# Kernel tuning notes

Hardware: AMD Instinct MI355X
Metric: run time of the kernel (lower is better)

The kernel has to match this reference:

```python
import jax, jax.numpy as jnp
import numpy as np

NEG_INF = -1.0e12  # matches torch's -1e12 mask value
LEAKY_SLOPE = 0.01  # nn.LeakyReLU default


def setup_inputs() -> dict:
    key = jax.random.key(0)
    k1, k2, k3, k4 = jax.random.split(key, 4)
    B, N, in_c, out_c = 8, 2048, 64, 64
    inp = jax.random.normal(k1, (B, N, in_c), dtype=jnp.float32)
    adj = jax.random.randint(k2, (B, N, N), 0, 2, dtype=jnp.int32)
    W = jax.random.normal(k3, (in_c, out_c), dtype=jnp.float32) * (1.0 / np.sqrt(in_c))
    a = jax.random.normal(k4, (2 * out_c, 1), dtype=jnp.float32) * 0.1
    return {"inp": inp, "adj": adj, "W": W, "a": a}


def reference(inp, adj, W, a):
    # GAT layer. The original builds an O(B*N^2*2*out_c) concat tensor;
    # a^T [h_i || h_j] decomposes exactly into (h_i . a1) + (h_j . a2).
    out_c = W.shape[1]
    h = jnp.einsum('bni,io->bno', inp, W)          # [B,N,out_c]
    a1 = a[:out_c, 0]                               # [out_c]
    a2 = a[out_c:, 0]                               # [out_c]
    e_i = h @ a1                                    # [B,N] source term
    e_j = h @ a2                                    # [B,N] target term
    e = e_i[:, :, None] + e_j[:, None, :]           # [B,N,N]
    e = jnp.where(e > 0, e, LEAKY_SLOPE * e)        # LeakyReLU(0.01)
    masked = jnp.where(adj > 0, e, NEG_INF)
    attention = jax.nn.softmax(masked, axis=2)      # [B,N,N]
    # dropout omitted (eval mode / deterministic reference)
    h_prime = jnp.einsum('bnm,bmo->bno', attention, h)  # [B,N,out_c]
    return h_prime
```

## Files before the change

kernel.cpp:

```cpp
#include <hip/hip_runtime.h>
#include <cstdint>

#define BB 8
#define NN 2048
#define CC 64
#define TI 64
#define JCH 128
#define NCH 8

typedef __attribute__((ext_vector_type(8))) _Float16 f16x8;
typedef __attribute__((ext_vector_type(4))) float f32x4;
typedef __attribute__((ext_vector_type(4))) unsigned int u32x4;
typedef __attribute__((ext_vector_type(4))) int i32x4;

static const size_t WS_H   = 0;
static const size_t WS_E1  = WS_H  + (size_t)BB*NN*CC;
static const size_t WS_E2  = WS_E1 + (size_t)BB*NN;
static const size_t WS_HT  = WS_E2 + (size_t)BB*NN;

#define GL16(g, l) __builtin_amdgcn_global_load_lds( \
    (const __attribute__((address_space(1))) void*)(g), \
    (__attribute__((address_space(3))) void*)(uint32_t)(uintptr_t)(l), 16, 0, 0)
#define GL4(g, l) __builtin_amdgcn_global_load_lds( \
    (const __attribute__((address_space(1))) void*)(g), \
    (__attribute__((address_space(3))) void*)(uint32_t)(uintptr_t)(l), 4, 0, 0)
#define WAIT14() asm volatile("s_waitcnt vmcnt(14)" ::: "memory")
#define WAIT0()  asm volatile("s_waitcnt vmcnt(0)" ::: "memory")
#define BAR()    __builtin_amdgcn_s_barrier()

__global__ __launch_bounds__(256) void k1_proj(const float* __restrict__ inp,
        const float* __restrict__ Wm, const float* __restrict__ av,
        float* __restrict__ h, float* __restrict__ e1, float* __restrict__ e2) {
    __shared__ float inp_lds[256];
    int t = threadIdx.x;
    size_t base = (size_t)blockIdx.x * 256;
    inp_lds[t] = inp[base + t];
    __syncthreads();
    int r = t >> 6;
    int c = t & 63;
    const float* irow = &inp_lds[r * 64];
    float acc = 0.f;
    #pragma unroll
    for (int k = 0; k < 64; k++) acc = fmaf(irow[k], Wm[k * 64 + c], acc);
    size_t row = (size_t)blockIdx.x * 4 + r;
    h[row * 64 + c] = acc;
    float v1 = acc * av[c];
    float v2 = acc * av[64 + c];
    #pragma unroll
    for (int o = 32; o > 0; o >>= 1) {
        v1 += __shfl_down(v1, o);
        v2 += __shfl_down(v2, o);
    }
    if (c == 0) { e1[row] = v1; e2[row] = v2; }
}

__global__ __launch_bounds__(256) void k1b_transpose(const float* __restrict__ h,
        unsigned short* __restrict__ hT) {
    __shared__ float tile[64][65];
    int t = threadIdx.x;
    int b = blockIdx.x >> 5;
    int i0 = (blockIdx.x & 31) * 64;
    const float* hb = h + ((size_t)b * NN + i0) * CC;
    #pragma unroll
    for (int q = 0; q < 16; q++) {
        int idx = q * 256 + t;
        tile[idx >> 6][idx & 63] = hb[idx];
    }
    __syncthreads();
    int c = t & 63;
    int rgrp = t >> 6;
    unsigned int uh[8];
    #pragma unroll
    for (int p = 0; p < 8; p++) {
        unsigned int pack_h = 0;
        #pragma unroll
        for (int s = 0; s < 2; s++) {
            float v = tile[rgrp * 16 + p * 2 + s][c];
            _Float16 fh = (_Float16)v;
            unsigned int u = (unsigned int)__builtin_bit_cast(unsigned short, fh);
            pack_h |= u << (16 * s);
        }
        uh[p] = pack_h;
    }
    size_t off = ((size_t)b * 64 + c) * NN + i0 + rgrp * 16;
    u32x4* dh = (u32x4*)(hT + off);
    dh[0] = u32x4{uh[0], uh[1], uh[2], uh[3]};
    dh[1] = u32x4{uh[4], uh[5], uh[6], uh[7]};
}

__global__ __launch_bounds__(512, 1) void k2_mfma(const int* __restrict__ adj,
        const unsigned short* __restrict__ hT,
        const float* __restrict__ e1, const float* __restrict__ e2,
        float* __restrict__ out) {
    __shared__ __align__(16) char smem[84224];

    int bid = blockIdx.x;
    int b    = bid & 7;
    int tile = bid >> 3;
    int i0 = tile * TI;

    int t = threadIdx.x;
    int w = t >> 6;
    int hw = w >> 2;
    int wl = w & 3;
    int l = t & 63;
    int col = l & 15;
    int kg  = l >> 4;
    int jbase = hw * 1024;

    int sl  = l & 15;
    int half_off = hw * 32768;

    const int* adjrow = adj + ((size_t)b * NN + i0 + wl * 16 + col) * NN;
    float e1v = e1[(size_t)b * NN + i0 + wl * 16 + col];
    const float* e2b = e2 + (size_t)b * NN;
    const unsigned short* hTb = hT + (size_t)b * 64 * NN;

    f32x4 acc[4];
    #pragma unroll
    for (int n = 0; n < 4; n++) acc[n] = f32x4{0.f, 0.f, 0.f, 0.f};
    f32x4 accZ = f32x4{0.f, 0.f, 0.f, 0.f};

    _Float16 onev = (_Float16)1.0f, zerov = (_Float16)0.0f;
    f16x8 onesf;
    #pragma unroll
    for (int i = 0; i < 8; i++) onesf[i] = (col == 0) ? onev : zerov;

    i32x4 aA[8], aB[8];

#define STAGE(jcN, B) { \
    int j0s = jbase + (jcN) * JCH; \
    char* lb = smem + half_off + ((B) ? 16384 : 0) + wl * 4096; \
    _Pragma("unroll") \
    for (int q = 0; q < 4; q++) { \
        int c = wl * 16 + q * 4 + (l >> 4); \
        const unsigned short* src = hTb + (size_t)c * NN + j0s + ((sl ^ (c & 7)) << 3); \
        GL16(src, lb + q * 1024); \
    } \
    char* e2d = smem + 65536 + hw * 1024 + ((B) ? 512 : 0); \
    GL4(e2b + j0s + l, e2d); \
    GL4(e2b + j0s + 64 + l, e2d + 256); \
}

#define ADJP(jcN, arr) { \
    int j0a = jbase + (jcN) * JCH; \
    _Pragma("unroll") \
    for (int ks = 0; ks < 4; ks++) { \
        const i32x4* ap = (const i32x4*)(adjrow + j0a + ks * 32 + kg * 8); \
        arr[2 * ks]     = ap[0]; \
        arr[2 * ks + 1] = ap[1]; \
    } \
}

#define COMPUTE(B, arr) { \
    const char* hLb = smem + half_off + ((B) ? 16384 : 0); \
    const float* e2c = (const float*)(smem + 65536 + hw * 1024 + ((B) ? 512 : 0)); \
    _Pragma("unroll") \
    for (int ks = 0; ks < 4; ks++) { \
        int krel = ks * 32 + kg * 8; \
        i32x4 a0 = arr[2 * ks]; \
        i32x4 a1 = arr[2 * ks + 1]; \
        f32x4 e20 = *(const f32x4*)(e2c + krel); \
        f32x4 e21 = *(const f32x4*)(e2c + krel + 4); \
        float xs[8] = {e20.x, e20.y, e20.z, e20.w, e21.x, e21.y, e21.z, e21.w}; \
        int ms[8] = {a0.x, a0.y, a0.z, a0.w, a1.x, a1.y, a1.z, a1.w}; \
        f16x8 pf; \
        _Pragma("unroll") \
        for (int i = 0; i < 8; i++) { \
            float x = e1v + xs[i]; \
            x = fmaxf(x, 0.01f * x); \
            x = __expf(x); \
            x = (ms[i] > 0) ? x : 0.0f; \
            pf[i] = (_Float16)x; \
        } \
        int seg = ks * 4 + kg; \
        _Pragma("unroll") \
        for (int n = 0; n < 4; n++) { \
            int c = n * 16 + col; \
            int boff = c * 256 + ((seg ^ (c & 7)) << 4); \
            f16x8 hv = __builtin_bit_cast(f16x8, *(const f32x4*)(hLb + boff)); \
            acc[n] = __builtin_amdgcn_mfma_f32_16x16x32_f16(pf, hv, acc[n], 0, 0, 0); \
        } \
        accZ = __builtin_amdgcn_mfma_f32_16x16x32_f16(pf, onesf, accZ, 0, 0, 0); \
    } \
}

    STAGE(0, 0);
    ADJP(0, aA);

    #pragma unroll
    for (int jc = 0; jc < NCH; jc += 2) {
        STAGE(jc + 1, 1);
        ADJP(jc + 1, aB);
        WAIT14();
        BAR();
        COMPUTE(0, aA);
        BAR();
        if (jc + 2 < NCH) {
            STAGE(jc + 2, 0);
            ADJP(jc + 2, aA);
            WAIT14();
        } else {
            WAIT0();
        }
        BAR();
        COMPUTE(1, aB);
        BAR();
    }

    float* red  = (float*)(smem + 67584 + wl * 4096);
    float* zred = (float*)(smem + 83968);
    if (hw == 1) {
        #pragma unroll
        for (int n = 0; n < 4; n++)
            #pragma unroll
            for (int r = 0; r < 4; r++)
                red[(kg * 4 + r) * 64 + n * 16 + col] = acc[n][r];
        if (col == 0) {
            #pragma unroll
            for (int r = 0; r < 4; r++) zred[wl * 16 + kg * 4 + r] = accZ[r];
        }
    }
    BAR();
    if (hw == 0 && col == 0) {
        #pragma unroll
        for (int r = 0; r < 4; r++) {
            float zt = accZ[r] + zred[wl * 16 + kg * 4 + r];
            zred[wl * 16 + kg * 4 + r] = (zt > 0.f) ? 1.0f / zt : 0.f;
        }
    }
    BAR();
    if (hw == 0) {
        float* outb = out + ((size_t)b * NN + i0 + wl * 16) * CC;
        #pragma unroll
        for (int r = 0; r < 4; r++) {
            float zi = zred[wl * 16 + kg * 4 + r];
            #pragma unroll
            for (int n = 0; n < 4; n++) {
                float v = (acc[n][r] + red[(kg * 4 + r) * 64 + n * 16 + col]) * zi;
                outb[(size_t)(kg * 4 + r) * CC + n * 16 + col] = v;
            }
        }
    }
#undef STAGE
#undef ADJP
#undef COMPUTE
}

extern "C" void kernel_launch(void* const* d_in, const int* in_sizes, int n_in,
                              void* d_out, int out_size, void* d_ws, size_t ws_size,
                              hipStream_t stream) {
    const float* inp = (const float*)d_in[0];
    const int*   adj = (const int*)d_in[1];
    const float* Wm  = (const float*)d_in[2];
    const float* av  = (const float*)d_in[3];
    float* ws = (float*)d_ws;
    float* h    = ws + WS_H;
    float* e1   = ws + WS_E1;
    float* e2   = ws + WS_E2;
    unsigned short* hT = (unsigned short*)(ws + WS_HT);
    float* out  = (float*)d_out;

    k1_proj<<<BB * NN / 4, 256, 0, stream>>>(inp, Wm, av, h, e1, e2);
    k1b_transpose<<<BB * (NN / 64), 256, 0, stream>>>(h, hT);
    k2_mfma<<<BB * (NN / TI), 512, 0, stream>>>(adj, hT, e1, e2, out);
}
```

Baseline: 48.35 us.

## Preload whole hT half into LDS, split J across blocks, add reduction kernel

The attention kernel now handles 128 rows per block with each of 8 waves owning 16 rows. It splits the key dimension across two blocks, each loading its full 1024-column half of hT and e2 into 128KB of LDS once up front. This removes the per-chunk staging barriers and double-buffering, and halves how often hT is re-read per row. Partial numerators and denominators go to workspace, and a new fourth kernel sums them and normalises. The cost is an extra launch plus partial-sum traffic, larger LDS use, and no overlap of the initial bulk load with compute.

```diff
diff --git a/kernel.cpp b/kernel.cpp
--- a/kernel.cpp
+++ b/kernel.cpp
@@ -4,9 +4,11 @@
 #define BB 8
 #define NN 2048
 #define CC 64
-#define TI 64
+#define TI 128
+#define JSPLIT 2
+#define KRANGE (NN / JSPLIT)
 #define JCH 128
-#define NCH 8
+#define NCH (KRANGE / JCH)
 
 typedef __attribute__((ext_vector_type(8))) _Float16 f16x8;
 typedef __attribute__((ext_vector_type(4))) float f32x4;
@@ -17,6 +19,8 @@
 static const size_t WS_E1  = WS_H  + (size_t)BB*NN*CC;
 static const size_t WS_E2  = WS_E1 + (size_t)BB*NN;
 static const size_t WS_HT  = WS_E2 + (size_t)BB*NN;
+static const size_t WS_ACC = WS_HT + (size_t)BB*CC*NN/2;
+static const size_t WS_Z   = WS_ACC + (size_t)JSPLIT*BB*NN*CC;
 
 #define GL16(g, l) __builtin_amdgcn_global_load_lds( \
     (const __attribute__((address_space(1))) void*)(g), \
@@ -24,7 +28,6 @@
 #define GL4(g, l) __builtin_amdgcn_global_load_lds( \
     (const __attribute__((address_space(1))) void*)(g), \
     (__attribute__((address_space(3))) void*)(uint32_t)(uintptr_t)(l), 4, 0, 0)
-#define WAIT14() asm volatile("s_waitcnt vmcnt(14)" ::: "memory")
 #define WAIT0()  asm volatile("s_waitcnt vmcnt(0)" ::: "memory")
 #define BAR()    __builtin_amdgcn_s_barrier()
 
@@ -91,28 +94,26 @@
 __global__ __launch_bounds__(512, 1) void k2_mfma(const int* __restrict__ adj,
         const unsigned short* __restrict__ hT,
         const float* __restrict__ e1, const float* __restrict__ e2,
-        float* __restrict__ out) {
-    __shared__ __align__(16) char smem[84224];
+        float* __restrict__ accp, float* __restrict__ zp) {
+    __shared__ __align__(16) char smem[135168];
+    float* e2L = (float*)(smem + 131072);
 
     int bid = blockIdx.x;
     int b    = bid & 7;
-    int tile = bid >> 3;
+    int rest = bid >> 3;
+    int s    = rest & 1;
+    int tile = rest >> 1;
     int i0 = tile * TI;
+    int jbase = s * KRANGE;
 
     int t = threadIdx.x;
     int w = t >> 6;
-    int hw = w >> 2;
-    int wl = w & 3;
     int l = t & 63;
     int col = l & 15;
     int kg  = l >> 4;
-    int jbase = hw * 1024;
-
-    int sl  = l & 15;
-    int half_off = hw * 32768;
-
-    const int* adjrow = adj + ((size_t)b * NN + i0 + wl * 16 + col) * NN;
-    float e1v = e1[(size_t)b * NN + i0 + wl * 16 + col];
+
+    const int* adjrow = adj + ((size_t)b * NN + i0 + w * 16 + col) * NN + jbase;
+    float e1v = e1[(size_t)b * NN + i0 + w * 16 + col];
     const float* e2b = e2 + (size_t)b * NN;
     const unsigned short* hTb = hT + (size_t)b * 64 * NN;
 
@@ -128,40 +129,24 @@
 
     i32x4 aA[8], aB[8];
 
-#define STAGE(jcN, B) { \
-    int j0s = jbase + (jcN) * JCH; \
-    char* lb = smem + half_off + ((B) ? 16384 : 0) + wl * 4096; \
+#define ADJP(jcN, arr) { \
     _Pragma("unroll") \
     for (int q = 0; q < 4; q++) { \
-        int c = wl * 16 + q * 4 + (l >> 4); \
-        const unsigned short* src = hTb + (size_t)c * NN + j0s + ((sl ^ (c & 7)) << 3); \
-        GL16(src, lb + q * 1024); \
+        const i32x4* ap = (const i32x4*)(adjrow + (jcN) * JCH + q * 32 + kg * 8); \
+        arr[2 * q]     = ap[0]; \
+        arr[2 * q + 1] = ap[1]; \
     } \
-    char* e2d = smem + 65536 + hw * 1024 + ((B) ? 512 : 0); \
-    GL4(e2b + j0s + l, e2d); \
-    GL4(e2b + j0s + 64 + l, e2d + 256); \
-}
-
-#define ADJP(jcN, arr) { \
-    int j0a = jbase + (jcN) * JCH; \
+}
+
+#define COMPUTE(jcN, arr) { \
     _Pragma("unroll") \
-    for (int ks = 0; ks < 4; ks++) { \
-        const i32x4* ap = (const i32x4*)(adjrow + j0a + ks * 32 + kg * 8); \
-        arr[2 * ks]     = ap[0]; \
-        arr[2 * ks + 1] = ap[1]; \
-    } \
-}
-
-#define COMPUTE(B, arr) { \
-    const char* hLb = smem + half_off + ((B) ? 16384 : 0); \
-    const float* e2c = (const float*)(smem + 65536 + hw * 1024 + ((B) ? 512 : 0)); \
-    _Pragma("unroll") \
-    for (int ks = 0; ks < 4; ks++) { \
+    for (int ks4 = 0; ks4 < 4; ks4++) { \
+        int ks = (jcN) * 4 + ks4; \
         int krel = ks * 32 + kg * 8; \
-        i32x4 a0 = arr[2 * ks]; \
-        i32x4 a1 = arr[2 * ks + 1]; \
-        f32x4 e20 = *(const f32x4*)(e2c + krel); \
-        f32x4 e21 = *(const f32x4*)(e2c + krel + 4); \
+        i32x4 a0 = arr[2 * ks4]; \
+        i32x4 a1 = arr[2 * ks4 + 1]; \
+        f32x4 e20 = *(const f32x4*)(e2L + krel); \
+        f32x4 e21 = *(const f32x4*)(e2L + krel + 4); \
         float xs[8] = {e20.x, e20.y, e20.z, e20.w, e21.x, e21.y, e21.z, e21.w}; \
         int ms[8] = {a0.x, a0.y, a0.z, a0.w, a1.x, a1.y, a1.z, a1.w}; \
         f16x8 pf; \
@@ -173,78 +158,78 @@
             x = (ms[i] > 0) ? x : 0.0f; \
             pf[i] = (_Float16)x; \
         } \
-        int seg = ks * 4 + kg; \
+        int g = ks * 4 + kg; \
         _Pragma("unroll") \
         for (int n = 0; n < 4; n++) { \
             int c = n * 16 + col; \
-            int boff = c * 256 + ((seg ^ (c & 7)) << 4); \
-            f16x8 hv = __builtin_bit_cast(f16x8, *(const f32x4*)(hLb + boff)); \
+            int p = (g & 120) | ((g ^ c) & 7); \
+            f16x8 hv = __builtin_bit_cast(f16x8, *(const f32x4*)(smem + c * 2048 + p * 16)); \
             acc[n] = __builtin_amdgcn_mfma_f32_16x16x32_f16(pf, hv, acc[n], 0, 0, 0); \
         } \
         accZ = __builtin_amdgcn_mfma_f32_16x16x32_f16(pf, onesf, accZ, 0, 0, 0); \
     } \
 }
 
-    STAGE(0, 0);
     ADJP(0, aA);
 
     #pragma unroll
+    for (int it = 0; it < 16; it++) {
+        int k16 = it * 8 + w;
+        int c   = k16 >> 1;
+        int p   = (k16 & 1) * 64 + l;
+        int g   = (p & 120) | ((p ^ c) & 7);
+        const unsigned short* src = hTb + (size_t)c * NN + jbase + g * 8;
+        GL16(src, smem + (size_t)k16 * 1024);
+    }
+    #pragma unroll
+    for (int it = 0; it < 2; it++) {
+        GL4(e2b + jbase + it * 512 + w * 64 + l,
+            smem + 131072 + (it * 512 + w * 64) * 4);
+    }
+    WAIT0();
+    BAR();
+
+    #pragma unroll
     for (int jc = 0; jc < NCH; jc += 2) {
-        STAGE(jc + 1, 1);
         ADJP(jc + 1, aB);
-        WAIT14();
-        BAR();
-        COMPUTE(0, aA);
-        BAR();
-        if (jc + 2 < NCH) {
-            STAGE(jc + 2, 0);
-            ADJP(jc + 2, aA);
-            WAIT14();
-        } else {
-            WAIT0();
-        }
-        BAR();
-        COMPUTE(1, aB);
-        BAR();
-    }
-
-    float* red  = (float*)(smem + 67584 + wl * 4096);
-    float* zred = (float*)(smem + 83968);
-    if (hw == 1) {
-        #pragma unroll
-        for (int n = 0; n < 4; n++)
-            #pragma unroll
-            for (int r = 0; r < 4; r++)
-                red[(kg * 4 + r) * 64 + n * 16 + col] = acc[n][r];
-        if (col == 0) {
-            #pragma unroll
-            for (int r = 0; r < 4; r++) zred[wl * 16 + kg * 4 + r] = accZ[r];
-        }
-    }
-    BAR();
-    if (hw == 0 && col == 0) {
+        COMPUTE(jc, aA);
+        if (jc + 2 < NCH) ADJP(jc + 2, aA);
+        COMPUTE(jc + 1, aB);
+    }
+
+    size_t orow = (size_t)s * BB * NN + (size_t)b * NN + i0 + w * 16 + kg * 4;
+    float* accout = accp + orow * CC;
+    #pragma unroll
+    for (int n = 0; n < 4; n++) {
         #pragma unroll
         for (int r = 0; r < 4; r++) {
-            float zt = accZ[r] + zred[wl * 16 + kg * 4 + r];
-            zred[wl * 16 + kg * 4 + r] = (zt > 0.f) ? 1.0f / zt : 0.f;
+            accout[(size_t)r * CC + n * 16 + col] = acc[n][r];
         }
     }
-    BAR();
-    if (hw == 0) {
-        float* outb = out + ((size_t)b * NN + i0 + wl * 16) * CC;
+    if (col == 0) {
         #pragma unroll
-        for (int r = 0; r < 4; r++) {
-            float zi = zred[wl * 16 + kg * 4 + r];
-            #pragma unroll
-            for (int n = 0; n < 4; n++) {
-                float v = (acc[n][r] + red[(kg * 4 + r) * 64 + n * 16 + col]) * zi;
-                outb[(size_t)(kg * 4 + r) * CC + n * 16 + col] = v;
-            }
-        }
-    }
-#undef STAGE
+        for (int r = 0; r < 4; r++) zp[orow + r] = accZ[r];
+    }
 #undef ADJP
 #undef COMPUTE
+}
+
+__global__ __launch_bounds__(256) void k3_final(const float* __restrict__ accp,
+        const float* __restrict__ zp, float* __restrict__ out) {
+    int idx = blockIdx.x * 256 + threadIdx.x;
+    const int TOT4 = BB * NN * CC / 4;
+    if (idx >= TOT4) return;
+    int row = idx >> 4;
+    f32x4 s0 = ((const f32x4*)accp)[idx];
+    f32x4 s1 = ((const f32x4*)accp)[idx + TOT4];
+    float z = zp[row] + zp[row + BB * NN];
+    float inv = (z > 0.f) ? (1.0f / z) : 0.f;
+    f32x4 o;
+    o.x = (s0.x + s1.x) * inv;
+    o.y = (s0.y + s1.y) * inv;
+    o.z = (s0.z + s1.z) * inv;
+    o.w = (s0.w + s1.w) * inv;
+    ((f32x4*)out)[idx] = o;
 }
 
 extern "C" void kernel_launch(void* const* d_in, const int* in_sizes, int n_in,
@@ -259,9 +244,12 @@
     float* e1   = ws + WS_E1;
     float* e2   = ws + WS_E2;
     unsigned short* hT = (unsigned short*)(ws + WS_HT);
+    float* accp = ws + WS_ACC;
+    float* zp   = ws + WS_Z;
     float* out  = (float*)d_out;
 
     k1_proj<<<BB * NN / 4, 256, 0, stream>>>(inp, Wm, av, h, e1, e2);
     k1b_transpose<<<BB * (NN / 64), 256, 0, stream>>>(h, hT);
-    k2_mfma<<<BB * (NN / TI), 512, 0, stream>>>(adj, hT, e1, e2, out);
-}
+    k2_mfma<<<BB * (NN / TI) * JSPLIT, 512, 0, stream>>>(adj, hT, e1, e2, accp, zp);
+    k3_final<<<(BB * NN * CC / 4 + 255) / 256, 256, 0, stream>>>(accp, zp, out);
+}
```

After: 44.89 us. -7.2%, faster.
